# Optimization experiments

Hardware: AMD Instinct MI355X
Metric: run time of the kernel (lower is better)

The kernel has to match this reference:

```python
import jax, jax.numpy as jnp
import numpy as np
from jax import lax

B, C, O, H, W = 32, 128, 256, 56, 56
BN_EPS = 1e-5
DW_THR = 4.0     # cut_conv2_3_DW threshold
PW_THR = 1e-3    # cut_conv2_3_PW threshold


def setup_inputs() -> dict:
    key = jax.random.key(0)
    ks = jax.random.split(key, 8)
    x = jax.random.normal(ks[0], (B, C, H, W), jnp.float32)
    # depthwise conv params: groups=C -> weight [C,1,3,3]
    dw_w = jax.random.normal(ks[1], (C, 1, 3, 3), jnp.float32) * 0.3
    dw_b = jax.random.normal(ks[2], (C,), jnp.float32) * 0.1
    dw_gamma = jnp.ones((C,), jnp.float32) + 0.1 * jax.random.normal(ks[3], (C,), jnp.float32)
    dw_beta = 0.1 * jax.random.normal(ks[4], (C,), jnp.float32)
    dw_mean = jnp.zeros((C,), jnp.float32)
    dw_var = jnp.ones((C,), jnp.float32)
    # pointwise 1x1 conv: weight [O,C,1,1] -> stored as [O,C]
    pw_w = jax.random.normal(ks[5], (O, C), jnp.float32) * 0.05
    pw_b = jax.random.normal(ks[6], (O,), jnp.float32) * 0.1
    pw_gamma = jnp.ones((O,), jnp.float32) + 0.1 * jax.random.normal(ks[7], (O,), jnp.float32)
    pw_beta = jnp.zeros((O,), jnp.float32)
    pw_mean = jnp.zeros((O,), jnp.float32)
    pw_var = jnp.ones((O,), jnp.float32)
    return {"x": x, "dw_w": dw_w, "dw_b": dw_b, "dw_gamma": dw_gamma,
            "dw_beta": dw_beta, "dw_mean": dw_mean, "dw_var": dw_var,
            "pw_w": pw_w, "pw_b": pw_b, "pw_gamma": pw_gamma,
            "pw_beta": pw_beta, "pw_mean": pw_mean, "pw_var": pw_var}


def _bn(x, gamma, beta, mean, var):
    scale = (gamma * lax.rsqrt(var + BN_EPS))[None, :, None, None]
    shift = (beta - mean * gamma * lax.rsqrt(var + BN_EPS))[None, :, None, None]
    return x * scale + shift


def _channel_cut(x, thr):
    # zero the full HxW plane of any (sample, channel) whose abs-max < thr
    maxabs = jnp.max(jnp.abs(x), axis=(2, 3), keepdims=True)  # [B,C',1,1]
    return jnp.where(maxabs < thr, jnp.zeros_like(x), x)


def reference(x, dw_w, dw_b, dw_gamma, dw_beta, dw_mean, dw_var,
              pw_w, pw_b, pw_gamma, pw_beta, pw_mean, pw_var):
    # depthwise 3x3 conv, padding=1, groups=C
    y = lax.conv_general_dilated(
        x, dw_w, window_strides=(1, 1), padding=((1, 1), (1, 1)),
        dimension_numbers=("NCHW", "OIHW", "NCHW"), feature_group_count=C)
    y = y + dw_b[None, :, None, None]
    y = jax.nn.relu(_bn(y, dw_gamma, dw_beta, dw_mean, dw_var))
    y = _channel_cut(y, DW_THR)
    # pointwise 1x1 conv == channel-mixing GEMM
    z = jnp.einsum("bchw,oc->bohw", y, pw_w) + pw_b[None, :, None, None]
    z = jax.nn.relu(_bn(z, pw_gamma, pw_beta, pw_mean, pw_var))
    z = _channel_cut(z, PW_THR)
    return z
```

## Files before the change

### kernel.cpp

```cpp
#include <hip/hip_runtime.h>
#include <math.h>

#define BB 32
#define CC 128
#define OO 256
#define HWSZ 3136
#define BN_EPS 1e-5f
#define DW_THR 4.0f

typedef __attribute__((ext_vector_type(8))) short short8;
typedef __attribute__((ext_vector_type(4))) short short4v;
typedef __attribute__((ext_vector_type(4))) float f32x4;

__device__ __forceinline__ unsigned bf16rne(float v) {
    unsigned u = __builtin_bit_cast(unsigned, v);
    return (u + 0x7fffu + ((u >> 16) & 1u)) >> 16;
}
__device__ __forceinline__ unsigned pack2(float a, float b) {
    return bf16rne(a) | (bf16rne(b) << 16);
}

__global__ __launch_bounds__(256) void prep_kernel(
    const float* __restrict__ pw_w, const float* __restrict__ pw_b,
    const float* __restrict__ pw_gamma, const float* __restrict__ pw_beta,
    const float* __restrict__ pw_mean, const float* __restrict__ pw_var,
    unsigned short* __restrict__ wb, float* __restrict__ bias2)
{
    const int idx = blockIdx.x * 256 + threadIdx.x;
    const int o = idx >> 7;
    const float s = pw_gamma[o] * rsqrtf(pw_var[o] + BN_EPS);
    wb[idx] = (unsigned short)bf16rne(pw_w[idx] * s);
    if (idx < OO) {
        const float s2 = pw_gamma[idx] * rsqrtf(pw_var[idx] + BN_EPS);
        bias2[idx] = pw_b[idx] * s2 + pw_beta[idx] - pw_mean[idx] * s2;
    }
}

__global__ __launch_bounds__(256) void dw_kernel(
    const float* __restrict__ x, const float* __restrict__ dw_w,
    const float* __restrict__ dw_b, const float* __restrict__ dw_gamma,
    const float* __restrict__ dw_beta, const float* __restrict__ dw_mean,
    const float* __restrict__ dw_var, unsigned short* __restrict__ y)
{
    const int cg = blockIdx.x;
    const int b  = blockIdx.y;
    const int tid = threadIdx.x;
    const int c0 = cg * 4;

    float wk[4][9], sc[4], bi[4];
#pragma unroll
    for (int c = 0; c < 4; ++c) {
        const int ch = c0 + c;
#pragma unroll
        for (int j = 0; j < 9; ++j) wk[c][j] = dw_w[ch * 9 + j];
        const float s = dw_gamma[ch] * rsqrtf(dw_var[ch] + BN_EPS);
        sc[c] = s;
        bi[c] = dw_b[ch] * s + dw_beta[ch] - dw_mean[ch] * s;
    }

    float vals[4][4][4];
    float cmax[4] = {0.f, 0.f, 0.f, 0.f};

#pragma unroll
    for (int is = 0; is < 4; ++is) {
        const int s = tid + is * 256;
        if (s < 784) {
            const int r  = s / 14;
            const int m  = s - r * 14;
            const int q4 = m * 4;
#pragma unroll
            for (int c = 0; c < 4; ++c) {
                const float* px = x + ((size_t)(b * CC + c0 + c)) * HWSZ;
                float a0 = 0.f, a1 = 0.f, a2 = 0.f, a3 = 0.f;
#pragma unroll
                for (int dr = 0; dr < 3; ++dr) {
                    const int rr = r + dr - 1;
                    const bool vr2 = (rr >= 0) && (rr < 56);
                    const float* prow = px + rr * 56 + q4;
                    float4 M = vr2 ? *(const float4*)prow
                                   : make_float4(0.f, 0.f, 0.f, 0.f);
                    float xm = (vr2 && m > 0)  ? prow[-1] : 0.f;
                    float xp = (vr2 && m < 13) ? prow[4]  : 0.f;
                    const float w0 = wk[c][dr*3+0];
                    const float w1 = wk[c][dr*3+1];
                    const float w2 = wk[c][dr*3+2];
                    a0 += w0*xm  + w1*M.x + w2*M.y;
                    a1 += w0*M.x + w1*M.y + w2*M.z;
                    a2 += w0*M.y + w1*M.z + w2*M.w;
                    a3 += w0*M.z + w1*M.w + w2*xp;
                }
                float v0 = fmaxf(a0*sc[c]+bi[c], 0.f);
                float v1 = fmaxf(a1*sc[c]+bi[c], 0.f);
                float v2 = fmaxf(a2*sc[c]+bi[c], 0.f);
                float v3 = fmaxf(a3*sc[c]+bi[c], 0.f);
                vals[is][c][0] = v0; vals[is][c][1] = v1;
                vals[is][c][2] = v2; vals[is][c][3] = v3;
                cmax[c] = fmaxf(cmax[c], fmaxf(fmaxf(v0, v1), fmaxf(v2, v3)));
            }
        }
    }

#pragma unroll
    for (int c = 0; c < 4; ++c)
#pragma unroll
        for (int off = 32; off; off >>= 1)
            cmax[c] = fmaxf(cmax[c], __shfl_xor(cmax[c], off, 64));
    __shared__ float smax[4][4];
    if ((tid & 63) == 0) {
#pragma unroll
        for (int c = 0; c < 4; ++c) smax[tid >> 6][c] = cmax[c];
    }
    __syncthreads();
    float f[4];
#pragma unroll
    for (int c = 0; c < 4; ++c) {
        float mx = fmaxf(fmaxf(smax[0][c], smax[1][c]),
                         fmaxf(smax[2][c], smax[3][c]));
        f[c] = (mx < DW_THR) ? 0.f : 1.f;
    }

    unsigned short* yp = y + ((size_t)(b * 32 + cg)) * HWSZ * 4;
#pragma unroll
    for (int is = 0; is < 4; ++is) {
        const int s = tid + is * 256;
        if (s < 784) {
            uint4 p0, p1;
            p0.x = pack2(vals[is][0][0]*f[0], vals[is][1][0]*f[1]);
            p0.y = pack2(vals[is][2][0]*f[2], vals[is][3][0]*f[3]);
            p0.z = pack2(vals[is][0][1]*f[0], vals[is][1][1]*f[1]);
            p0.w = pack2(vals[is][2][1]*f[2], vals[is][3][1]*f[3]);
            p1.x = pack2(vals[is][0][2]*f[0], vals[is][1][2]*f[1]);
            p1.y = pack2(vals[is][2][2]*f[2], vals[is][3][2]*f[3]);
            p1.z = pack2(vals[is][0][3]*f[0], vals[is][1][3]*f[1]);
            p1.w = pack2(vals[is][2][3]*f[2], vals[is][3][3]*f[3]);
            *(uint4*)(yp + (size_t)s * 16)     = p0;
            *(uint4*)(yp + (size_t)s * 16 + 8) = p1;
        }
    }
}

__global__ __launch_bounds__(256) void pw_kernel(
    const unsigned short* __restrict__ yt,
    const unsigned short* __restrict__ wb,
    const float* __restrict__ bias2,
    float* __restrict__ out)
{
    const int nt = blockIdx.x;
    const int b  = blockIdx.y;
    const int n0 = nt * 64;
    const int tid = threadIdx.x;
    const int w   = tid >> 6;
    const int l   = tid & 63;
    const int g   = l >> 4;
    const int lan = l & 15;

    __shared__ unsigned short Ys[32 * 64 * 4];

    const unsigned short* ysrc = yt + (size_t)b * (32 * HWSZ * 4);
#pragma unroll
    for (int i = 0; i < 4; ++i) {
        const int q  = tid + 256 * i;
        const int cg = q >> 5;
        const int rr = q & 31;
        const uint4 v = *(const uint4*)(ysrc + (size_t)cg * (HWSZ * 4)
                                        + n0 * 4 + rr * 8);
        *(uint4*)(Ys + q * 8) = v;
    }
    __syncthreads();

    f32x4 acc[4][4] = {};

#pragma unroll
    for (int kk = 0; kk < 4; ++kk) {
        short8 a[4];
#pragma unroll
        for (int mr = 0; mr < 4; ++mr)
            a[mr] = *(const short8*)(wb + (size_t)(w*64 + mr*16 + lan) * CC
                                     + kk*32 + g*8);
#pragma unroll
        for (int nr = 0; nr < 4; ++nr) {
            const int base = (kk*8 + 2*g) * 256 + (nr*16 + lan) * 4;
            short4v lo = *(const short4v*)(Ys + base);
            short4v hi = *(const short4v*)(Ys + base + 256);
            short8 bf = __builtin_shufflevector(lo, hi, 0,1,2,3,4,5,6,7);
#pragma unroll
            for (int mr = 0; mr < 4; ++mr)
                acc[mr][nr] = __builtin_amdgcn_mfma_f32_16x16x32_bf16(
                    a[mr], bf, acc[mr][nr], 0, 0, 0);
        }
    }

    float* zb = out + ((size_t)b * OO) * HWSZ + n0;
#pragma unroll
    for (int mr = 0; mr < 4; ++mr) {
#pragma unroll
        for (int reg = 0; reg < 4; ++reg) {
            const int o = w*64 + mr*16 + g*4 + reg;
            const float bv = bias2[o];
            float* zo = zb + (size_t)o * HWSZ;
#pragma unroll
            for (int nr = 0; nr < 4; ++nr) {
                float val = fmaxf(acc[mr][nr][reg] + bv, 0.f);
                zo[nr*16 + lan] = val;
            }
        }
    }
}

extern "C" void kernel_launch(void* const* d_in, const int* in_sizes, int n_in,
                              void* d_out, int out_size, void* d_ws, size_t ws_size,
                              hipStream_t stream)
{
    const float* x        = (const float*)d_in[0];
    const float* dw_w     = (const float*)d_in[1];
    const float* dw_b     = (const float*)d_in[2];
    const float* dw_gamma = (const float*)d_in[3];
    const float* dw_beta  = (const float*)d_in[4];
    const float* dw_mean  = (const float*)d_in[5];
    const float* dw_var   = (const float*)d_in[6];
    const float* pw_w     = (const float*)d_in[7];
    const float* pw_b     = (const float*)d_in[8];
    const float* pw_gamma = (const float*)d_in[9];
    const float* pw_beta  = (const float*)d_in[10];
    const float* pw_mean  = (const float*)d_in[11];
    const float* pw_var   = (const float*)d_in[12];

    unsigned short* yws  = (unsigned short*)d_ws;
    unsigned short* wbuf = (unsigned short*)((char*)d_ws + 25690112);
    float*          b2   = (float*)((char*)d_ws + 25690112 + 65536);

    prep_kernel<<<128, 256, 0, stream>>>(pw_w, pw_b, pw_gamma, pw_beta,
                                         pw_mean, pw_var, wbuf, b2);

    dim3 g1(32, 32);
    dw_kernel<<<g1, 256, 0, stream>>>(x, dw_w, dw_b, dw_gamma, dw_beta,
                                      dw_mean, dw_var, yws);

    dim3 g2(49, 32);
    pw_kernel<<<g2, 256, 0, stream>>>(yws, wbuf, b2, (float*)d_out);
}
```

Baseline: 200.0 us.

## Defer DW channel cut to pointwise GEMM via mask, swap MFMA operands

The depthwise kernel now writes bf16 activations straight away instead of holding all values in registers until the block-wide max is known. It emits a per-(batch, 4-channel-group) 16-bit mask that the pointwise kernel ANDs into the loaded activations. The pointwise kernel drops its LDS staging and reads activations directly from global memory as the MFMA A operand. Weights become the B operand, so the output can be stored as float4 along the spatial dimension. This cuts register pressure in the depthwise kernel and removes LDS traffic and the barrier, at the cost of uncoalesced 8-byte global loads in the GEMM.

```diff
diff --git a/kernel.cpp b/kernel.cpp
--- a/kernel.cpp
+++ b/kernel.cpp
@@ -5,12 +5,14 @@
 #define CC 128
 #define OO 256
 #define HWSZ 3136
+#define HW4 (HWSZ*4)
 #define BN_EPS 1e-5f
 #define DW_THR 4.0f
 
 typedef __attribute__((ext_vector_type(8))) short short8;
-typedef __attribute__((ext_vector_type(4))) short short4v;
 typedef __attribute__((ext_vector_type(4))) float f32x4;
+typedef __attribute__((ext_vector_type(4))) unsigned uint4v;
+typedef __attribute__((ext_vector_type(2))) unsigned uint2v;
 
 __device__ __forceinline__ unsigned bf16rne(float v) {
     unsigned u = __builtin_bit_cast(unsigned, v);
@@ -40,7 +42,8 @@
     const float* __restrict__ x, const float* __restrict__ dw_w,
     const float* __restrict__ dw_b, const float* __restrict__ dw_gamma,
     const float* __restrict__ dw_beta, const float* __restrict__ dw_mean,
-    const float* __restrict__ dw_var, unsigned short* __restrict__ y)
+    const float* __restrict__ dw_var, unsigned short* __restrict__ y,
+    uint2v* __restrict__ mask64)
 {
     const int cg = blockIdx.x;
     const int b  = blockIdx.y;
@@ -58,8 +61,8 @@
         bi[c] = dw_b[ch] * s + dw_beta[ch] - dw_mean[ch] * s;
     }
 
-    float vals[4][4][4];
     float cmax[4] = {0.f, 0.f, 0.f, 0.f};
+    unsigned short* yp = y + ((size_t)(b * 32 + cg)) * HW4;
 
 #pragma unroll
     for (int is = 0; is < 4; ++is) {
@@ -68,6 +71,7 @@
             const int r  = s / 14;
             const int m  = s - r * 14;
             const int q4 = m * 4;
+            float vals[4][4];
 #pragma unroll
             for (int c = 0; c < 4; ++c) {
                 const float* px = x + ((size_t)(b * CC + c0 + c)) * HWSZ;
@@ -93,10 +97,21 @@
                 float v1 = fmaxf(a1*sc[c]+bi[c], 0.f);
                 float v2 = fmaxf(a2*sc[c]+bi[c], 0.f);
                 float v3 = fmaxf(a3*sc[c]+bi[c], 0.f);
-                vals[is][c][0] = v0; vals[is][c][1] = v1;
-                vals[is][c][2] = v2; vals[is][c][3] = v3;
+                vals[c][0] = v0; vals[c][1] = v1;
+                vals[c][2] = v2; vals[c][3] = v3;
                 cmax[c] = fmaxf(cmax[c], fmaxf(fmaxf(v0, v1), fmaxf(v2, v3)));
             }
+            uint4 p0, p1;
+            p0.x = pack2(vals[0][0], vals[1][0]);
+            p0.y = pack2(vals[2][0], vals[3][0]);
+            p0.z = pack2(vals[0][1], vals[1][1]);
+            p0.w = pack2(vals[2][1], vals[3][1]);
+            p1.x = pack2(vals[0][2], vals[1][2]);
+            p1.y = pack2(vals[2][2], vals[3][2]);
+            p1.z = pack2(vals[0][3], vals[1][3]);
+            p1.w = pack2(vals[2][3], vals[3][3]);
+            *(uint4*)(yp + (size_t)s * 16)     = p0;
+            *(uint4*)(yp + (size_t)s * 16 + 8) = p1;
         }
     }
 
@@ -111,31 +126,18 @@
         for (int c = 0; c < 4; ++c) smax[tid >> 6][c] = cmax[c];
     }
     __syncthreads();
-    float f[4];
-#pragma unroll
-    for (int c = 0; c < 4; ++c) {
-        float mx = fmaxf(fmaxf(smax[0][c], smax[1][c]),
-                         fmaxf(smax[2][c], smax[3][c]));
-        f[c] = (mx < DW_THR) ? 0.f : 1.f;
-    }
-
-    unsigned short* yp = y + ((size_t)(b * 32 + cg)) * HWSZ * 4;
-#pragma unroll
-    for (int is = 0; is < 4; ++is) {
-        const int s = tid + is * 256;
-        if (s < 784) {
-            uint4 p0, p1;
-            p0.x = pack2(vals[is][0][0]*f[0], vals[is][1][0]*f[1]);
-            p0.y = pack2(vals[is][2][0]*f[2], vals[is][3][0]*f[3]);
-            p0.z = pack2(vals[is][0][1]*f[0], vals[is][1][1]*f[1]);
-            p0.w = pack2(vals[is][2][1]*f[2], vals[is][3][1]*f[3]);
-            p1.x = pack2(vals[is][0][2]*f[0], vals[is][1][2]*f[1]);
-            p1.y = pack2(vals[is][2][2]*f[2], vals[is][3][2]*f[3]);
-            p1.z = pack2(vals[is][0][3]*f[0], vals[is][1][3]*f[1]);
-            p1.w = pack2(vals[is][2][3]*f[2], vals[is][3][3]*f[3]);
-            *(uint4*)(yp + (size_t)s * 16)     = p0;
-            *(uint4*)(yp + (size_t)s * 16 + 8) = p1;
-        }
+    if (tid == 0) {
+        unsigned mw[4];
+#pragma unroll
+        for (int c = 0; c < 4; ++c) {
+            float mx = fmaxf(fmaxf(smax[0][c], smax[1][c]),
+                             fmaxf(smax[2][c], smax[3][c]));
+            mw[c] = (mx < DW_THR) ? 0u : 0xFFFFu;
+        }
+        uint2v mv;
+        mv.x = mw[0] | (mw[1] << 16);
+        mv.y = mw[2] | (mw[3] << 16);
+        mask64[b * 32 + cg] = mv;
     }
 }
 
@@ -143,66 +145,70 @@
     const unsigned short* __restrict__ yt,
     const unsigned short* __restrict__ wb,
     const float* __restrict__ bias2,
+    const uint2v* __restrict__ mask64,
     float* __restrict__ out)
 {
-    const int nt = blockIdx.x;
+    const int n0 = blockIdx.x * 64;
     const int b  = blockIdx.y;
-    const int n0 = nt * 64;
     const int tid = threadIdx.x;
-    const int w   = tid >> 6;
+    const int ow  = (tid >> 6) * 64;
     const int l   = tid & 63;
     const int g   = l >> 4;
     const int lan = l & 15;
 
-    __shared__ unsigned short Ys[32 * 64 * 4];
-
-    const unsigned short* ysrc = yt + (size_t)b * (32 * HWSZ * 4);
-#pragma unroll
-    for (int i = 0; i < 4; ++i) {
-        const int q  = tid + 256 * i;
-        const int cg = q >> 5;
-        const int rr = q & 31;
-        const uint4 v = *(const uint4*)(ysrc + (size_t)cg * (HWSZ * 4)
-                                        + n0 * 4 + rr * 8);
-        *(uint4*)(Ys + q * 8) = v;
-    }
-    __syncthreads();
+    const unsigned short* yb = yt + (size_t)b * (32 * HW4);
+
+    uint4v mk[4];
+    const uint2v* mb = mask64 + b * 32;
+#pragma unroll
+    for (int kk = 0; kk < 4; ++kk)
+        mk[kk] = *(const uint4v*)&mb[kk * 8 + 2 * g];
+
+    float bv[4];
+#pragma unroll
+    for (int orr = 0; orr < 4; ++orr)
+        bv[orr] = bias2[ow + orr * 16 + lan];
 
     f32x4 acc[4][4] = {};
 
 #pragma unroll
     for (int kk = 0; kk < 4; ++kk) {
-        short8 a[4];
-#pragma unroll
-        for (int mr = 0; mr < 4; ++mr)
-            a[mr] = *(const short8*)(wb + (size_t)(w*64 + mr*16 + lan) * CC
-                                     + kk*32 + g*8);
-#pragma unroll
-        for (int nr = 0; nr < 4; ++nr) {
-            const int base = (kk*8 + 2*g) * 256 + (nr*16 + lan) * 4;
-            short4v lo = *(const short4v*)(Ys + base);
-            short4v hi = *(const short4v*)(Ys + base + 256);
-            short8 bf = __builtin_shufflevector(lo, hi, 0,1,2,3,4,5,6,7);
-#pragma unroll
-            for (int mr = 0; mr < 4; ++mr)
-                acc[mr][nr] = __builtin_amdgcn_mfma_f32_16x16x32_bf16(
-                    a[mr], bf, acc[mr][nr], 0, 0, 0);
-        }
-    }
-
-    float* zb = out + ((size_t)b * OO) * HWSZ + n0;
+        short8 bfr[4];
+#pragma unroll
+        for (int orr = 0; orr < 4; ++orr)
+            bfr[orr] = *(const short8*)(wb
+                + (size_t)(ow + orr * 16 + lan) * CC + kk * 32 + g * 8);
+#pragma unroll
+        for (int mr = 0; mr < 4; ++mr) {
+            const unsigned short* ya = yb + (size_t)(kk * 8 + 2 * g) * HW4
+                                       + (size_t)(n0 + mr * 16 + lan) * 4;
+            uint2v lo = *(const uint2v*)ya;
+            uint2v hi = *(const uint2v*)(ya + HW4);
+            uint4v w4;
+            w4.x = lo.x & mk[kk].x;
+            w4.y = lo.y & mk[kk].y;
+            w4.z = hi.x & mk[kk].z;
+            w4.w = hi.y & mk[kk].w;
+            const short8 a = __builtin_bit_cast(short8, w4);
+#pragma unroll
+            for (int orr = 0; orr < 4; ++orr)
+                acc[mr][orr] = __builtin_amdgcn_mfma_f32_16x16x32_bf16(
+                    a, bfr[orr], acc[mr][orr], 0, 0, 0);
+        }
+    }
+
 #pragma unroll
     for (int mr = 0; mr < 4; ++mr) {
 #pragma unroll
-        for (int reg = 0; reg < 4; ++reg) {
-            const int o = w*64 + mr*16 + g*4 + reg;
-            const float bv = bias2[o];
-            float* zo = zb + (size_t)o * HWSZ;
-#pragma unroll
-            for (int nr = 0; nr < 4; ++nr) {
-                float val = fmaxf(acc[mr][nr][reg] + bv, 0.f);
-                zo[nr*16 + lan] = val;
-            }
+        for (int orr = 0; orr < 4; ++orr) {
+            const int o = ow + orr * 16 + lan;
+            float4 r;
+            r.x = fmaxf(acc[mr][orr][0] + bv[orr], 0.f);
+            r.y = fmaxf(acc[mr][orr][1] + bv[orr], 0.f);
+            r.z = fmaxf(acc[mr][orr][2] + bv[orr], 0.f);
+            r.w = fmaxf(acc[mr][orr][3] + bv[orr], 0.f);
+            *(float4*)&out[((size_t)b * OO + o) * HWSZ
+                           + n0 + mr * 16 + g * 4] = r;
         }
     }
 }
@@ -228,14 +234,15 @@
     unsigned short* yws  = (unsigned short*)d_ws;
     unsigned short* wbuf = (unsigned short*)((char*)d_ws + 25690112);
     float*          b2   = (float*)((char*)d_ws + 25690112 + 65536);
+    uint2v*         msk  = (uint2v*)((char*)d_ws + 25690112 + 65536 + 1024);
 
     prep_kernel<<<128, 256, 0, stream>>>(pw_w, pw_b, pw_gamma, pw_beta,
                                          pw_mean, pw_var, wbuf, b2);
 
     dim3 g1(32, 32);
     dw_kernel<<<g1, 256, 0, stream>>>(x, dw_w, dw_b, dw_gamma, dw_beta,
-                                      dw_mean, dw_var, yws);
+                                      dw_mean, dw_var, yws, msk);
 
     dim3 g2(49, 32);
-    pw_kernel<<<g2, 256, 0, stream>>>(yws, wbuf, b2, (float*)d_out);
-}
+    pw_kernel<<<g2, 256, 0, stream>>>(yws, wbuf, b2, msk, (float*)d_out);
+}
```

New measurement: 204.3 us. 1.02x slower.
